# Kernel tuning notes

Measured on AMD Instinct MI355X. Metric: run time of the kernel, lower is better.

## Reference

```python
import jax, jax.numpy as jnp
import numpy as np

D_MODEL = 256
NHEAD = 8
DK = D_MODEL // NHEAD
EDGE_FEAT_DIM = 7
N_NODES = 2048
N_EDGES = 65536
LN_EPS = 1e-5


def _ln(x, g, b):
    mu = jnp.mean(x, axis=-1, keepdims=True)
    var = jnp.mean(jnp.square(x - mu), axis=-1, keepdims=True)
    return (x - mu) * jax.lax.rsqrt(var + LN_EPS) * g + b


def setup_inputs() -> dict:
    key = jax.random.key(0)
    ks = jax.random.split(key, 16)
    d, h2 = D_MODEL, 2 * D_MODEL
    s = 0.02
    inp = {
        "h": jax.random.normal(ks[0], (N_NODES, d), jnp.float32),
        "edge_attr": jax.random.normal(ks[1], (N_EDGES, EDGE_FEAT_DIM), jnp.float32),
        # weights stored as (in, out): y = x @ W + b (matches torch Linear math)
        "Wq": s * jax.random.normal(ks[2], (d, d), jnp.float32),
        "bq": jnp.zeros((d,), jnp.float32),
        "Wk": s * jax.random.normal(ks[3], (d, d), jnp.float32),
        "bk": jnp.zeros((d,), jnp.float32),
        "Wv": s * jax.random.normal(ks[4], (d, d), jnp.float32),
        "bv": jnp.zeros((d,), jnp.float32),
        "Wo": s * jax.random.normal(ks[5], (d, d), jnp.float32),
        "bo": jnp.zeros((d,), jnp.float32),
        "We": s * jax.random.normal(ks[6], (EDGE_FEAT_DIM, NHEAD), jnp.float32),
        "be": jnp.zeros((NHEAD,), jnp.float32),
        "ln1_g": jnp.ones((d,), jnp.float32),
        "ln1_b": jnp.zeros((d,), jnp.float32),
        "fln_g": jnp.ones((d,), jnp.float32),
        "fln_b": jnp.zeros((d,), jnp.float32),
        "W1": s * jax.random.normal(ks[7], (d, h2), jnp.float32),
        "b1": jnp.zeros((h2,), jnp.float32),
        "W2": s * jax.random.normal(ks[8], (h2, d), jnp.float32),
        "b2": jnp.zeros((d,), jnp.float32),
        "edge_index": jax.random.randint(ks[9], (2, N_EDGES), 0, N_NODES, jnp.int64 if jax.config.jax_enable_x64 else jnp.int32),
    }
    return inp


def reference(h, edge_attr, Wq, bq, Wk, bk, Wv, bv, Wo, bo, We, be,
              ln1_g, ln1_b, fln_g, fln_b, W1, b1, W2, b2, edge_index):
    N = h.shape[0]
    res = h
    # edge bias scattered into dense (N, N, H) tensor
    eb = edge_attr @ We + be                                  # (E, H)
    attn_bias = jnp.zeros((N, N, NHEAD), h.dtype).at[edge_index[0], edge_index[1]].set(eb)
    Q = (h @ Wq + bq).reshape(N, NHEAD, DK)
    K = (h @ Wk + bk).reshape(N, NHEAD, DK)
    V = (h @ Wv + bv).reshape(N, NHEAD, DK)
    scores = jnp.einsum('nhd,mhd->nmh', Q, K) / jnp.sqrt(jnp.float32(DK)) + attn_bias
    attn = jax.nn.softmax(scores, axis=1)                     # softmax over keys m
    out = jnp.einsum('nmh,mhd->nhd', attn, V).reshape(N, D_MODEL)
    out = out @ Wo + bo
    h1 = _ln(res + out, ln1_g, ln1_b)
    ffn = jax.nn.gelu(_ln(h1, fln_g, fln_b) @ W1 + b1, approximate=False) @ W2 + b2
    return h1 + ffn
```

## Files before the change

### kernel.cpp

```cpp
#include <hip/hip_runtime.h>
#include <math.h>

#define NN 2048
#define NE 65536
#define DM 256
#define NH 8
#define DKH 32
#define CAP 128
#define TM2 128
#define SPLIT 4

typedef __attribute__((ext_vector_type(8))) short bf16x8;
typedef __attribute__((ext_vector_type(4))) float f32x4;

#define WAVE_LDS_SYNC() __asm__ volatile("s_waitcnt lgkmcnt(0)" ::: "memory")

__device__ __forceinline__ unsigned short f2b(float f) {
    unsigned u = __float_as_uint(f);
    unsigned r = (u + 0x7FFFu + ((u >> 16) & 1u)) >> 16;
    return (unsigned short)r;
}
__device__ __forceinline__ float b2f(unsigned short s) {
    return __uint_as_float(((unsigned)s) << 16);
}

__global__ __launch_bounds__(256) void prep_all_kernel(
    const float* __restrict__ h, const float* __restrict__ Wq,
    const float* __restrict__ Wk, const float* __restrict__ Wv,
    const float* __restrict__ Wo, const float* __restrict__ W1,
    const float* __restrict__ W2, const float* __restrict__ ea,
    const float* __restrict__ We, const float* __restrict__ be,
    const int* __restrict__ ei,
    unsigned short* __restrict__ hb, unsigned short* __restrict__ Wqkvt,
    unsigned short* __restrict__ Wot, unsigned short* __restrict__ W1t,
    unsigned short* __restrict__ W2t, float* __restrict__ eb,
    int* __restrict__ cnt, int* __restrict__ lst)
{
    int b = blockIdx.x;
    if (b < 4096) {
        int i = b * 256 + threadIdx.x;
        if (i < 524288) {
            hb[i] = f2b(h[i]);
        } else if (i < 720896) {
            int j = i - 524288;
            int n = j >> 8, k = j & 255;
            const float* W = (n < 256) ? Wq : (n < 512) ? Wk : Wv;
            Wqkvt[j] = f2b(W[k * 256 + (n & 255)]);
        } else if (i < 786432) {
            int j = i - 720896;
            int n = j >> 8, k = j & 255;
            Wot[j] = f2b(Wo[k * 256 + n]);
        } else if (i < 917504) {
            int j = i - 786432;
            int n = j >> 8, k = j & 255;
            W1t[j] = f2b(W1[(size_t)k * 512 + n]);
        } else {
            int j = i - 917504;
            int n = j >> 9, k = j & 511;
            W2t[j] = f2b(W2[(size_t)k * 256 + n]);
        }
    } else {
        int e = (b - 4096) * 256 + threadIdx.x;
        float acc[NH];
#pragma unroll
        for (int hh = 0; hh < NH; ++hh) acc[hh] = be[hh];
#pragma unroll
        for (int f = 0; f < 7; ++f) {
            float x = ea[e * 7 + f];
#pragma unroll
            for (int hh = 0; hh < NH; ++hh) acc[hh] = fmaf(x, We[f * NH + hh], acc[hh]);
        }
#pragma unroll
        for (int hh = 0; hh < NH; ++hh)
            eb[e * NH + hh] = acc[hh] * 1.44269504088896f;
        int s = ei[e];
        int p = atomicAdd(&cnt[s], 1);
        if (p < CAP) lst[s * CAP + p] = e;
    }
}

__global__ __launch_bounds__(128) void rowprep_kernel(
    const int* __restrict__ ei, const int* __restrict__ cnt,
    const int* __restrict__ lst, int* __restrict__ sortedDest,
    int* __restrict__ sortedE, int* __restrict__ rowOff)
{
    __shared__ int ds[CAP], es[CAP];
    __shared__ int bc[16], off[17];
    int n = blockIdx.x, t = threadIdx.x;
    int c = cnt[n]; if (c > CAP) c = CAP;
    if (t < 16) bc[t] = 0;
    int e = -1, d = -1;
    if (t < c) { e = lst[n * CAP + t]; d = ei[NE + e]; }
    ds[t] = d; es[t] = e;
    __syncthreads();
    bool win = (t < c);
    if (win) {
        for (int j = 0; j < c; ++j)
            if (ds[j] == d && es[j] > e) { win = false; break; }
    }
    int bkt = (d >= 0) ? (d >> 7) : 0;
    int pos = -1;
    if (win) pos = atomicAdd(&bc[bkt], 1);
    __syncthreads();
    if (t == 0) {
        int s = 0;
        for (int i = 0; i < 16; ++i) { off[i] = s; s += bc[i]; }
        off[16] = s;
    }
    __syncthreads();
    if (win) {
        int p = off[bkt] + pos;
        sortedDest[n * CAP + p] = d;
        sortedE[n * CAP + p] = e;
    }
    if (t < 17) rowOff[n * 17 + t] = off[t];
}

template <int EPI, int MT>
__global__ __launch_bounds__(MT * 4) void gemm_bf16(
    const unsigned short* __restrict__ A, const unsigned short* __restrict__ Bt,
    const float* __restrict__ bias0, const float* __restrict__ bias1,
    const float* __restrict__ bias2, const float* __restrict__ resid,
    void* __restrict__ out0, void* __restrict__ out1, void* __restrict__ out2,
    int M, int N, int K)
{
    __shared__ unsigned short As[MT][40];
    __shared__ unsigned short Bs[64][40];
    int tid = threadIdx.x;
    int wv = tid >> 6, l = tid & 63, l15 = l & 15, quad = l >> 4;
    int m0 = blockIdx.y * MT, n0 = blockIdx.x * 64;

    f32x4 acc[4];
#pragma unroll
    for (int i = 0; i < 4; ++i) acc[i] = (f32x4){0.f, 0.f, 0.f, 0.f};

    int ra = tid >> 2, ka = (tid & 3) * 8;

    for (int k0 = 0; k0 < K; k0 += 32) {
        *(uint4*)&As[ra][ka] = *(const uint4*)(A + (size_t)(m0 + ra) * K + k0 + ka);
        if (MT == 64) {
            *(uint4*)&Bs[ra][ka] = *(const uint4*)(Bt + (size_t)(n0 + ra) * K + k0 + ka);
        } else {
            int rb = tid >> 1, kb = (tid & 1) * 16;
            *(uint4*)&Bs[rb][kb]     = *(const uint4*)(Bt + (size_t)(n0 + rb) * K + k0 + kb);
            *(uint4*)&Bs[rb][kb + 8] = *(const uint4*)(Bt + (size_t)(n0 + rb) * K + k0 + kb + 8);
        }
        __syncthreads();
        bf16x8 a = *(const bf16x8*)&As[wv * 16 + l15][quad * 8];
#pragma unroll
        for (int nt = 0; nt < 4; ++nt) {
            bf16x8 b = *(const bf16x8*)&Bs[nt * 16 + l15][quad * 8];
            acc[nt] = __builtin_amdgcn_mfma_f32_16x16x32_bf16(a, b, acc[nt], 0, 0, 0);
        }
        __syncthreads();
    }

#pragma unroll
    for (int nt = 0; nt < 4; ++nt) {
#pragma unroll
        for (int r = 0; r < 4; ++r) {
            int row = m0 + wv * 16 + quad * 4 + r;
            int col = n0 + nt * 16 + l15;
            float v = acc[nt][r];
            if (EPI == 0) {
                v += bias0[col];
                if (resid) v += resid[(size_t)row * N + col];
                ((float*)out0)[(size_t)row * N + col] = v;
            } else if (EPI == 1) {
                v += bias0[col];
                v = 0.5f * v * (1.0f + erff(v * 0.70710678118654752f));
                ((unsigned short*)out0)[(size_t)row * N + col] = f2b(v);
            } else {
                if (col < 256) {
                    v = (v + bias0[col]) * 0.2550348592f;
                    ((unsigned short*)out0)[(size_t)row * 256 + col] = f2b(v);
                } else if (col < 512) {
                    v += bias1[col - 256];
                    ((unsigned short*)out1)[(size_t)row * 256 + col - 256] = f2b(v);
                } else {
                    v += bias2[col - 512];
                    ((unsigned short*)out2)[(size_t)row * 256 + col - 512] = f2b(v);
                }
            }
        }
    }
}

__global__ __launch_bounds__(256) void vtrans_kernel(
    const unsigned short* __restrict__ Vb, unsigned short* __restrict__ Vt)
{
    __shared__ unsigned short tile[64][40];
    int h = blockIdx.y, n0 = blockIdx.x * 64, t = threadIdx.x;
    int r = t >> 2, c8 = (t & 3) * 8;
    *(uint4*)&tile[r][c8] = *(const uint4*)(Vb + (size_t)(n0 + r) * DM + h * 32 + c8);
    __syncthreads();
    int d = t >> 3, nc = (t & 7) * 8;
    unsigned short o[8];
#pragma unroll
    for (int j = 0; j < 8; ++j) o[j] = tile[nc + j][d];
    *(uint4*)(Vt + ((size_t)h * 32 + d) * NN + n0 + nc) = *(uint4*)o;
}

__global__ __launch_bounds__(256) void attn_mfma(
    const unsigned short* __restrict__ Qb, const unsigned short* __restrict__ Kb,
    const unsigned short* __restrict__ Vt, const float* __restrict__ eb,
    const int* __restrict__ sortedDest, const int* __restrict__ sortedE,
    const int* __restrict__ rowOff,
    float* __restrict__ accD, float* __restrict__ lD)
{
    __shared__ __align__(16) unsigned short Ks[TM2][40];
    __shared__ __align__(16) unsigned short Vs[32][TM2 + 8];
    __shared__ __align__(16) unsigned short Pn[4][16][TM2 + 16];
    __shared__ float ldelta[4][16];
    int h = blockIdx.y, tid = threadIdx.x;
    int wv = tid >> 6, l = tid & 63, l15 = l & 15, quad = l >> 4;
    int n0 = blockIdx.x * 64 + wv * 16;
    int mz = blockIdx.z;

    if (l < 16) ldelta[wv][l] = 0.f;

    bf16x8 aq = *(const bf16x8*)(Qb + (size_t)(n0 + l15) * DM + h * 32 + quad * 8);

    f32x4 oacc[2];
    oacc[0] = (f32x4){0.f, 0.f, 0.f, 0.f};
    oacc[1] = (f32x4){0.f, 0.f, 0.f, 0.f};
    float lacc = 0.f;
    const unsigned short* Vth = Vt + (size_t)h * 32 * NN;

    int r16 = l >> 2, sub = l & 3;
    int frow = n0 + r16;

    for (int t = 0; t < NN / (TM2 * SPLIT); ++t) {
        int m0 = (mz * (NN / SPLIT)) + t * TM2;
        int ti = m0 >> 7;
        {
            int r = tid >> 1, kc = (tid & 1) * 16;
            const unsigned short* ks = Kb + (size_t)(m0 + r) * DM + h * 32 + kc;
            *(uint4*)&Ks[r][kc]     = *(const uint4*)(ks);
            *(uint4*)&Ks[r][kc + 8] = *(const uint4*)(ks + 8);
            int d = tid >> 3, mc = (tid & 7) * 16;
            const unsigned short* vs = Vth + (size_t)d * NN + m0 + mc;
            *(uint4*)&Vs[d][mc]     = *(const uint4*)(vs);
            *(uint4*)&Vs[d][mc + 8] = *(const uint4*)(vs + 8);
        }
        __syncthreads();
#pragma unroll
        for (int mt = 0; mt < TM2 / 16; ++mt) {
            bf16x8 ak = *(const bf16x8*)&Ks[mt * 16 + l15][quad * 8];
            f32x4 s = __builtin_amdgcn_mfma_f32_16x16x32_bf16(
                ak, aq, (f32x4){0.f, 0.f, 0.f, 0.f}, 0, 0, 0);
            float p0 = __builtin_amdgcn_exp2f(s[0]);
            float p1 = __builtin_amdgcn_exp2f(s[1]);
            float p2 = __builtin_amdgcn_exp2f(s[2]);
            float p3 = __builtin_amdgcn_exp2f(s[3]);
            lacc += (p0 + p1) + (p2 + p3);
            unsigned u0 = (unsigned)f2b(p0) | ((unsigned)f2b(p1) << 16);
            unsigned u1 = (unsigned)f2b(p2) | ((unsigned)f2b(p3) << 16);
            *(uint2*)&Pn[wv][l15][mt * 16 + quad * 4] = (uint2){u0, u1};
        }
        WAVE_LDS_SYNC();
        {
            int o0 = rowOff[frow * 17 + ti];
            int o1 = rowOff[frow * 17 + ti + 1];
            for (int idx = o0 + sub; idx < o1; idx += 4) {
                int d = sortedDest[frow * CAP + idx] - m0;
                int e = sortedE[frow * CAP + idx];
                float expb = __builtin_amdgcn_exp2f(eb[e * NH + h]);
                float pold = b2f(Pn[wv][r16][d]);
                Pn[wv][r16][d] = f2b(pold * expb);
                atomicAdd(&ldelta[wv][r16], pold * (expb - 1.0f));
            }
        }
        WAVE_LDS_SYNC();
#pragma unroll
        for (int kc = 0; kc < TM2 / 32; ++kc) {
            bf16x8 ap = *(const bf16x8*)&Pn[wv][l15][kc * 32 + quad * 8];
#pragma unroll
            for (int nt = 0; nt < 2; ++nt) {
                bf16x8 bv = *(const bf16x8*)&Vs[nt * 16 + l15][kc * 32 + quad * 8];
                oacc[nt] = __builtin_amdgcn_mfma_f32_16x16x32_bf16(ap, bv, oacc[nt], 0, 0, 0);
            }
        }
        __syncthreads();
    }

    lacc += __shfl_xor(lacc, 16);
    lacc += __shfl_xor(lacc, 32);
    float* lDp = lD + (size_t)mz * NN * NH;
    if (l < 16)
        lDp[(size_t)(n0 + l) * NH + h] = lacc + ldelta[wv][l];
    float* aDp = accD + (size_t)mz * NN * DM;
#pragma unroll
    for (int nt = 0; nt < 2; ++nt)
#pragma unroll
        for (int r = 0; r < 4; ++r)
            aDp[(size_t)(n0 + quad * 4 + r) * DM + h * 32 + nt * 16 + l15] = oacc[nt][r];
}

__global__ __launch_bounds__(256) void wo_ln_kernel(
    const float* __restrict__ accD, const float* __restrict__ lD,
    const unsigned short* __restrict__ Wot, const float* __restrict__ bo,
    const float* __restrict__ h, const float* __restrict__ g1,
    const float* __restrict__ b1, const float* __restrict__ g2,
    const float* __restrict__ b2, float* __restrict__ H1,
    unsigned short* __restrict__ X2b)
{
    __shared__ float linv[16][8];
    __shared__ __align__(16) unsigned short As[16][264];
    __shared__ __align__(16) unsigned short Bs[256][40];
    __shared__ float Tt[16][264];
    __shared__ unsigned short X2s[16][264];
    int tid = threadIdx.x, m0 = blockIdx.x * 16;
    int wv = tid >> 6, l = tid & 63, l15 = l & 15, quad = l >> 4;

    if (tid < 128) {
        int r = tid >> 3, hh = tid & 7;
        float ls = 0.f;
#pragma unroll
        for (int s = 0; s < SPLIT; ++s)
            ls += lD[(size_t)s * NN * NH + (size_t)(m0 + r) * NH + hh];
        linv[r][hh] = 1.0f / ls;
    }
    __syncthreads();
#pragma unroll
    for (int ch = 0; ch < 16; ++ch) {
        float o = 0.f;
#pragma unroll
        for (int s = 0; s < SPLIT; ++s)
            o += accD[(size_t)s * NN * DM + (size_t)(m0 + ch) * DM + tid];
        As[ch][tid] = f2b(o * linv[ch][tid >> 5]);
    }
    __syncthreads();

    f32x4 acc[4];
#pragma unroll
    for (int i = 0; i < 4; ++i) acc[i] = (f32x4){0.f, 0.f, 0.f, 0.f};

    for (int k0 = 0; k0 < 256; k0 += 32) {
#pragma unroll
        for (int ps = 0; ps < 4; ++ps) {
            int row = ps * 64 + (tid >> 2), kk = (tid & 3) * 8;
            *(uint4*)&Bs[row][kk] = *(const uint4*)(Wot + (size_t)row * 256 + k0 + kk);
        }
        __syncthreads();
        bf16x8 a = *(const bf16x8*)&As[l15][k0 + quad * 8];
#pragma unroll
        for (int nt = 0; nt < 4; ++nt) {
            bf16x8 b = *(const bf16x8*)&Bs[wv * 64 + nt * 16 + l15][quad * 8];
            acc[nt] = __builtin_amdgcn_mfma_f32_16x16x32_bf16(a, b, acc[nt], 0, 0, 0);
        }
        __syncthreads();
    }

#pragma unroll
    for (int nt = 0; nt < 4; ++nt)
#pragma unroll
        for (int r = 0; r < 4; ++r) {
            int row = quad * 4 + r, col = wv * 64 + nt * 16 + l15;
            Tt[row][col] = acc[nt][r] + bo[col] + h[(size_t)(m0 + row) * DM + col];
        }
    __syncthreads();

    int rr = tid >> 4, l16 = tid & 15;
    float x[16];
#pragma unroll
    for (int j = 0; j < 16; ++j) x[j] = Tt[rr][l16 + 16 * j];
    float mu = 0.f;
#pragma unroll
    for (int j = 0; j < 16; ++j) mu += x[j];
#pragma unroll
    for (int off = 1; off < 16; off <<= 1) mu += __shfl_xor(mu, off);
    mu *= (1.0f / 256.0f);
    float var = 0.f;
#pragma unroll
    for (int j = 0; j < 16; ++j) { float d = x[j] - mu; var += d * d; }
#pragma unroll
    for (int off = 1; off < 16; off <<= 1) var += __shfl_xor(var, off);
    float rs = rsqrtf(var * (1.0f / 256.0f) + 1e-5f);
    float y[16]; float mu2 = 0.f;
#pragma unroll
    for (int j = 0; j < 16; ++j) {
        int c = l16 + 16 * j;
        y[j] = (x[j] - mu) * rs * g1[c] + b1[c];
        mu2 += y[j];
    }
#pragma unroll
    for (int off = 1; off < 16; off <<= 1) mu2 += __shfl_xor(mu2, off);
    mu2 *= (1.0f / 256.0f);
    float var2 = 0.f;
#pragma unroll
    for (int j = 0; j < 16; ++j) { float d = y[j] - mu2; var2 += d * d; }
#pragma unroll
    for (int off = 1; off < 16; off <<= 1) var2 += __shfl_xor(var2, off);
    float rs2 = rsqrtf(var2 * (1.0f / 256.0f) + 1e-5f);
#pragma unroll
    for (int j = 0; j < 16; ++j) {
        int c = l16 + 16 * j;
        Tt[rr][c] = y[j];
        X2s[rr][c] = f2b((y[j] - mu2) * rs2 * g2[c] + b2[c]);
    }
    __syncthreads();
#pragma unroll
    for (int ch = 0; ch < 16; ++ch) {
        H1[(size_t)(m0 + ch) * DM + tid] = Tt[ch][tid];
        X2b[(size_t)(m0 + ch) * DM + tid] = X2s[ch][tid];
    }
}

extern "C" void kernel_launch(void* const* d_in, const int* in_sizes, int n_in,
                              void* d_out, int out_size, void* d_ws, size_t ws_size,
                              hipStream_t stream)
{
    const float* h    = (const float*)d_in[0];
    const float* ea   = (const float*)d_in[1];
    const float* Wq   = (const float*)d_in[2];
    const float* bq   = (const float*)d_in[3];
    const float* Wk   = (const float*)d_in[4];
    const float* bk   = (const float*)d_in[5];
    const float* Wv   = (const float*)d_in[6];
    const float* bv   = (const float*)d_in[7];
    const float* Wo   = (const float*)d_in[8];
    const float* bo   = (const float*)d_in[9];
    const float* We   = (const float*)d_in[10];
    const float* be   = (const float*)d_in[11];
    const float* ln1g = (const float*)d_in[12];
    const float* ln1b = (const float*)d_in[13];
    const float* flng = (const float*)d_in[14];
    const float* flnb = (const float*)d_in[15];
    const float* W1   = (const float*)d_in[16];
    const float* b1   = (const float*)d_in[17];
    const float* W2   = (const float*)d_in[18];
    const float* b2   = (const float*)d_in[19];
    const int*   ei   = (const int*)d_in[20];
    float* out = (float*)d_out;

    char* p = (char*)d_ws;
    float* eb   = (float*)p;           p += (size_t)NE * NH * 4;
    int*   cnt  = (int*)p;             p += (size_t)NN * 4;
    int*   lst  = (int*)p;             p += (size_t)NN * CAP * 4;
    int*   sD   = (int*)p;             p += (size_t)NN * CAP * 4;
    int*   sE   = (int*)p;             p += (size_t)NN * CAP * 4;
    int*   rOff = (int*)p;             p += (size_t)NN * 17 * 4;
    unsigned short* hb    = (unsigned short*)p; p += (size_t)NN * DM * 2;
    unsigned short* Wqkvt = (unsigned short*)p; p += (size_t)768 * 256 * 2;
    unsigned short* Wot   = (unsigned short*)p; p += (size_t)256 * 256 * 2;
    unsigned short* W1t   = (unsigned short*)p; p += (size_t)512 * 256 * 2;
    unsigned short* W2t   = (unsigned short*)p; p += (size_t)256 * 512 * 2;
    unsigned short* Qb    = (unsigned short*)p; p += (size_t)NN * DM * 2;
    unsigned short* Kb    = (unsigned short*)p; p += (size_t)NN * DM * 2;
    unsigned short* Vb    = (unsigned short*)p; p += (size_t)NN * DM * 2;
    unsigned short* Vt    = (unsigned short*)p; p += (size_t)NN * DM * 2;
    float* accD = (float*)p;           p += (size_t)SPLIT * NN * DM * 4;
    float* lD   = (float*)p;           p += (size_t)SPLIT * NN * NH * 4;
    float* H1   = (float*)p;           p += (size_t)NN * DM * 4;
    unsigned short* X2b   = (unsigned short*)p; p += (size_t)NN * DM * 2;
    unsigned short* F1b   = (unsigned short*)p; p += (size_t)NN * 512 * 2;

    hipMemsetAsync(cnt, 0, (size_t)NN * 4, stream);
    prep_all_kernel<<<4096 + NE / 256, 256, 0, stream>>>(
        h, Wq, Wk, Wv, Wo, W1, W2, ea, We, be, ei,
        hb, Wqkvt, Wot, W1t, W2t, eb, cnt, lst);
    rowprep_kernel<<<NN, 128, 0, stream>>>(ei, cnt, lst, sD, sE, rOff);

    gemm_bf16<2, 64><<<dim3(768 / 64, NN / 64), 256, 0, stream>>>(
        hb, Wqkvt, bq, bk, bv, nullptr, Qb, Kb, Vb, NN, 768, 256);
    vtrans_kernel<<<dim3(NN / 64, NH), 256, 0, stream>>>(Vb, Vt);

    attn_mfma<<<dim3(NN / 64, NH, SPLIT), 256, 0, stream>>>(
        Qb, Kb, Vt, eb, sD, sE, rOff, accD, lD);

    wo_ln_kernel<<<NN / 16, 256, 0, stream>>>(
        accD, lD, Wot, bo, h, ln1g, ln1b, flng, flnb, H1, X2b);

    gemm_bf16<1, 64><<<dim3(512 / 64, NN / 64), 256, 0, stream>>>(
        X2b, W1t, b1, nullptr, nullptr, nullptr, F1b, nullptr, nullptr, NN, 512, 256);
    gemm_bf16<0, 32><<<dim3(256 / 64, NN / 32), 128, 0, stream>>>(
        F1b, W2t, b2, nullptr, nullptr, H1, out, nullptr, nullptr, NN, 256, 512);
}
```

Measured before the change: 179.0 us.

## Fuse V transpose into QKV GEMM epilogue and widen GEMM K-tile

```diff
diff --git a/kernel.cpp b/kernel.cpp
--- a/kernel.cpp
+++ b/kernel.cpp
@@ -124,8 +124,8 @@
     void* __restrict__ out0, void* __restrict__ out1, void* __restrict__ out2,
     int M, int N, int K)
 {
-    __shared__ unsigned short As[MT][40];
-    __shared__ unsigned short Bs[64][40];
+    __shared__ __align__(16) unsigned short As[MT][136];
+    __shared__ __align__(16) unsigned short Bs[64][136];
     int tid = threadIdx.x;
     int wv = tid >> 6, l = tid & 63, l15 = l & 15, quad = l >> 4;
     int m0 = blockIdx.y * MT, n0 = blockIdx.x * 64;
@@ -134,33 +134,61 @@
 #pragma unroll
     for (int i = 0; i < 4; ++i) acc[i] = (f32x4){0.f, 0.f, 0.f, 0.f};
 
-    int ra = tid >> 2, ka = (tid & 3) * 8;
-
-    for (int k0 = 0; k0 < K; k0 += 32) {
-        *(uint4*)&As[ra][ka] = *(const uint4*)(A + (size_t)(m0 + ra) * K + k0 + ka);
+    for (int k0 = 0; k0 < K; k0 += 128) {
         if (MT == 64) {
-            *(uint4*)&Bs[ra][ka] = *(const uint4*)(Bt + (size_t)(n0 + ra) * K + k0 + ka);
+            int row = tid >> 2, cb = (tid & 3) * 32;
+            const unsigned short* ap = A + (size_t)(m0 + row) * K + k0 + cb;
+#pragma unroll
+            for (int i = 0; i < 4; ++i)
+                *(uint4*)&As[row][cb + i * 8] = *(const uint4*)(ap + i * 8);
+            const unsigned short* bp = Bt + (size_t)(n0 + row) * K + k0 + cb;
+#pragma unroll
+            for (int i = 0; i < 4; ++i)
+                *(uint4*)&Bs[row][cb + i * 8] = *(const uint4*)(bp + i * 8);
         } else {
-            int rb = tid >> 1, kb = (tid & 1) * 16;
-            *(uint4*)&Bs[rb][kb]     = *(const uint4*)(Bt + (size_t)(n0 + rb) * K + k0 + kb);
-            *(uint4*)&Bs[rb][kb + 8] = *(const uint4*)(Bt + (size_t)(n0 + rb) * K + k0 + kb + 8);
-        }
-        __syncthreads();
-        bf16x8 a = *(const bf16x8*)&As[wv * 16 + l15][quad * 8];
-#pragma unroll
-        for (int nt = 0; nt < 4; ++nt) {
-            bf16x8 b = *(const bf16x8*)&Bs[nt * 16 + l15][quad * 8];
-            acc[nt] = __builtin_amdgcn_mfma_f32_16x16x32_bf16(a, b, acc[nt], 0, 0, 0);
+            int rowa = tid >> 2, cba = (tid & 3) * 32;
+            const unsigned short* ap = A + (size_t)(m0 + rowa) * K + k0 + cba;
+#pragma unroll
+            for (int i = 0; i < 4; ++i)
+                *(uint4*)&As[rowa][cba + i * 8] = *(const uint4*)(ap + i * 8);
+            int rowb = tid >> 1, cbb = (tid & 1) * 64;
+            const unsigned short* bp = Bt + (size_t)(n0 + rowb) * K + k0 + cbb;
+#pragma unroll
+            for (int i = 0; i < 8; ++i)
+                *(uint4*)&Bs[rowb][cbb + i * 8] = *(const uint4*)(bp + i * 8);
+        }
+        __syncthreads();
+#pragma unroll
+        for (int ks = 0; ks < 4; ++ks) {
+            bf16x8 a = *(const bf16x8*)&As[wv * 16 + l15][ks * 32 + quad * 8];
+#pragma unroll
+            for (int nt = 0; nt < 4; ++nt) {
+                bf16x8 b = *(const bf16x8*)&Bs[nt * 16 + l15][ks * 32 + quad * 8];
+                acc[nt] = __builtin_amdgcn_mfma_f32_16x16x32_bf16(a, b, acc[nt], 0, 0, 0);
+            }
         }
         __syncthreads();
     }
 
 #pragma unroll
     for (int nt = 0; nt < 4; ++nt) {
+        int colb = n0 + nt * 16;
+        if (EPI == 2 && colb >= 512) {
+            int n = colb + l15 - 512;
+            float bv = bias2[n];
+            unsigned short s0 = f2b(acc[nt][0] + bv);
+            unsigned short s1 = f2b(acc[nt][1] + bv);
+            unsigned short s2 = f2b(acc[nt][2] + bv);
+            unsigned short s3 = f2b(acc[nt][3] + bv);
+            uint2 pk = { (unsigned)s0 | ((unsigned)s1 << 16),
+                         (unsigned)s2 | ((unsigned)s3 << 16) };
+            *(uint2*)((unsigned short*)out2 + (size_t)n * NN + m0 + wv * 16 + quad * 4) = pk;
+            continue;
+        }
 #pragma unroll
         for (int r = 0; r < 4; ++r) {
             int row = m0 + wv * 16 + quad * 4 + r;
-            int col = n0 + nt * 16 + l15;
+            int col = colb + l15;
             float v = acc[nt][r];
             if (EPI == 0) {
                 v += bias0[col];
@@ -174,31 +202,13 @@
                 if (col < 256) {
                     v = (v + bias0[col]) * 0.2550348592f;
                     ((unsigned short*)out0)[(size_t)row * 256 + col] = f2b(v);
-                } else if (col < 512) {
+                } else {
                     v += bias1[col - 256];
                     ((unsigned short*)out1)[(size_t)row * 256 + col - 256] = f2b(v);
-                } else {
-                    v += bias2[col - 512];
-                    ((unsigned short*)out2)[(size_t)row * 256 + col - 512] = f2b(v);
                 }
             }
         }
     }
-}
-
-__global__ __launch_bounds__(256) void vtrans_kernel(
-    const unsigned short* __restrict__ Vb, unsigned short* __restrict__ Vt)
-{
-    __shared__ unsigned short tile[64][40];
-    int h = blockIdx.y, n0 = blockIdx.x * 64, t = threadIdx.x;
-    int r = t >> 2, c8 = (t & 3) * 8;
-    *(uint4*)&tile[r][c8] = *(const uint4*)(Vb + (size_t)(n0 + r) * DM + h * 32 + c8);
-    __syncthreads();
-    int d = t >> 3, nc = (t & 7) * 8;
-    unsigned short o[8];
-#pragma unroll
-    for (int j = 0; j < 8; ++j) o[j] = tile[nc + j][d];
-    *(uint4*)(Vt + ((size_t)h * 32 + d) * NN + n0 + nc) = *(uint4*)o;
 }
 
 __global__ __launch_bounds__(256) void attn_mfma(
@@ -448,7 +458,6 @@
     unsigned short* W2t   = (unsigned short*)p; p += (size_t)256 * 512 * 2;
     unsigned short* Qb    = (unsigned short*)p; p += (size_t)NN * DM * 2;
     unsigned short* Kb    = (unsigned short*)p; p += (size_t)NN * DM * 2;
-    unsigned short* Vb    = (unsigned short*)p; p += (size_t)NN * DM * 2;
     unsigned short* Vt    = (unsigned short*)p; p += (size_t)NN * DM * 2;
     float* accD = (float*)p;           p += (size_t)SPLIT * NN * DM * 4;
     float* lD   = (float*)p;           p += (size_t)SPLIT * NN * NH * 4;
@@ -463,8 +472,7 @@
     rowprep_kernel<<<NN, 128, 0, stream>>>(ei, cnt, lst, sD, sE, rOff);
 
     gemm_bf16<2, 64><<<dim3(768 / 64, NN / 64), 256, 0, stream>>>(
-        hb, Wqkvt, bq, bk, bv, nullptr, Qb, Kb, Vb, NN, 768, 256);
-    vtrans_kernel<<<dim3(NN / 64, NH), 256, 0, stream>>>(Vb, Vt);
+        hb, Wqkvt, bq, bk, bv, nullptr, Qb, Kb, Vt, NN, 768, 256);
 
     attn_mfma<<<dim3(NN / 64, NH, SPLIT), 256, 0, stream>>>(
         Qb, Kb, Vt, eb, sD, sE, rOff, accD, lD);
```

After: 171.7 us. 4.1% less time.
